# Performance work log

Measured on AMD Instinct MI355X. Metric: run time of the kernel, lower is better.

## Reference

```python
import jax, jax.numpy as jnp
import numpy as np
from jax import lax

B, GRID = 256, 58  # 28*2+2 per scn.InputLayer spatial size


def _conv(x, w):
    # x: [B,C,H,W], w: [O,C,k,k]; scn.Convolution is VALID, stride 1, no bias
    return lax.conv_general_dilated(
        x, w, window_strides=(1, 1), padding='VALID',
        dimension_numbers=('NCHW', 'OIHW', 'NCHW'))


def _maxpool2(x):
    return lax.reduce_window(x, -jnp.inf, lax.max,
                             window_dimensions=(1, 1, 2, 2),
                             window_strides=(1, 1, 2, 2), padding='VALID')


def setup_inputs() -> dict:
    key = jax.random.key(0)
    k0, k1, k2, k3, k4 = jax.random.split(key, 5)
    return {
        'x': jax.random.normal(k0, (B, 1, GRID, GRID), dtype=jnp.float32),
        'w1': jax.random.normal(k1, (64, 1, 5, 5), dtype=jnp.float32) * 0.1,
        'w2': jax.random.normal(k2, (128, 64, 5, 5), dtype=jnp.float32) * 0.025,
        'lw': jax.random.normal(k3, (10, 128), dtype=jnp.float32) * 0.09,
        'lb': jax.random.normal(k4, (10,), dtype=jnp.float32) * 0.01,
    }


def reference(x, w1, w2, lw, lb):
    h = _conv(x, w1)          # [B,64,54,54]
    h = _maxpool2(h)          # [B,64,27,27]
    h = _conv(h, w2)          # [B,128,23,23]
    h = jnp.transpose(h, (0, 2, 3, 1))  # channels-last for linear
    return jnp.einsum('bhwc,oc->bhwo', h, lw) + lb  # [B,23,23,10]
```

## Files before the change

kernel.cpp:

```cpp
#include <hip/hip_runtime.h>


typedef __attribute__((ext_vector_type(8))) short bf16x8;
typedef __attribute__((ext_vector_type(4))) float f32x4;
typedef __attribute__((ext_vector_type(4))) unsigned int u32x4;

#define MFMA16(a, b, c) __builtin_amdgcn_mfma_f32_16x16x32_bf16((a), (b), (c), 0, 0, 0)

static __device__ __forceinline__ unsigned short f2bf(float f) {
    unsigned u = __builtin_bit_cast(unsigned, f);
    u += 0x7FFFu + ((u >> 16) & 1u);
    return (unsigned short)(u >> 16);
}

__global__ __launch_bounds__(256) void prep_w2c(
    const float* __restrict__ w2, unsigned short* __restrict__ w2c)
{
    int t = blockIdx.x * 256 + threadIdx.x;
    if (t >= 25600) return;
    const int lane = t & 63, khalf = (t >> 6) & 1, nt = (t >> 7) & 7, kk = t >> 10;
    const int l16 = lane & 15, kg = lane >> 4;
    const int oc = nt * 16 + l16;
    const int icb = khalf * 32 + kg * 8;
    unsigned pk[4];
#pragma unroll
    for (int h = 0; h < 4; ++h) {
        unsigned short lo = f2bf(w2[oc * 1600 + (icb + 2 * h) * 25 + kk]);
        unsigned short hi = f2bf(w2[oc * 1600 + (icb + 2 * h + 1) * 25 + kk]);
        pk[h] = (unsigned)lo | ((unsigned)hi << 16);
    }
    u32x4 v; v.x = pk[0]; v.y = pk[1]; v.z = pk[2]; v.w = pk[3];
    *(u32x4*)(w2c + (size_t)t * 8) = v;
}

#define XBF_OFF  104976
#define W1T_OFF  111704
#define ECON_STR 272
#define LWT_OFF  147968
#define LDS_TOT  152320

__global__ __launch_bounds__(512, 2) void fused_net(
    const float* __restrict__ x, const float* __restrict__ w1,
    const unsigned short* __restrict__ w2c,
    const float* __restrict__ lw, const float* __restrict__ lb,
    float* __restrict__ out)
{
    extern __shared__ char lds[];
    unsigned short* xbf = (unsigned short*)(lds + XBF_OFF);
    unsigned short* w1t = (unsigned short*)(lds + W1T_OFF);
    const int b = blockIdx.x, tid = threadIdx.x;
    const int lane = tid & 63, w = tid >> 6;
    const int l16 = lane & 15, kg = lane >> 4;
    const int ocg = w & 1, mg = w >> 1;
    const int mstart = (mg == 0) ? 0 : mg * 8 + 1;

    const float4* xg = (const float4*)(x + b * 3364);
    for (int i = tid; i < 841; i += 512) {
        float4 v = xg[i];
        unsigned p0 = (unsigned)f2bf(v.x) | ((unsigned)f2bf(v.y) << 16);
        unsigned p1 = (unsigned)f2bf(v.z) | ((unsigned)f2bf(v.w) << 16);
        *(uint2*)(xbf + i * 4) = make_uint2(p0, p1);
    }
    for (int i = tid; i < 2048; i += 512) {
        int k = i >> 6, oc = i & 63;
        w1t[i] = (k < 25) ? f2bf(w1[oc * 25 + k]) : (unsigned short)0;
    }
    for (int i = tid; i < 2048; i += 512) {
        int o = i >> 7, cc = i & 127;
        float v = (o < 10) ? lw[o * 128 + cc] : 0.f;
        *(unsigned short*)(lds + LWT_OFF + o * 272 + cc * 2) = f2bf(v);
    }
    __syncthreads();

    {
        int koff[8];
        unsigned kmsk[8];
#pragma unroll
        for (int j = 0; j < 8; ++j) {
            int k = kg * 8 + j;
            int kh = k / 5, kw = k - 5 * kh;
            koff[j] = (k < 25) ? (kh * 58 + kw) : 0;
            kmsk[j] = (k < 25) ? 0xFFFFu : 0u;
        }
        bf16x8 bfrag[4];
#pragma unroll
        for (int ot = 0; ot < 4; ++ot)
#pragma unroll
            for (int j = 0; j < 8; ++j)
                bfrag[ot][j] = (short)w1t[(kg * 8 + j) * 64 + ot * 16 + l16];

        const f32x4 zero4 = {0.f, 0.f, 0.f, 0.f};
        for (int t = w; t < 183; t += 8) {
            int p = t * 4 + (l16 >> 2);
            if (p > 728) p = 728;
            const int q = l16 & 3;
            const int ph = p / 27, pw = p - 27 * ph;
            const int base = (2 * ph + (q >> 1)) * 58 + 2 * pw + (q & 1);
            bf16x8 afrag;
#pragma unroll
            for (int j = 0; j < 8; ++j)
                afrag[j] = (short)(xbf[base + koff[j]] & kmsk[j]);
            f32x4 acc1[4];
#pragma unroll
            for (int ot = 0; ot < 4; ++ot)
                acc1[ot] = MFMA16(afrag, bfrag[ot], zero4);
            const int pout = t * 4 + kg;
            if (pout < 729) {
#pragma unroll
                for (int ot = 0; ot < 4; ++ot) {
                    float m = fmaxf(fmaxf(acc1[ot][0], acc1[ot][1]),
                                    fmaxf(acc1[ot][2], acc1[ot][3]));
                    *(unsigned short*)(lds + pout * 144 + (ot * 16 + l16) * 2)
                        = f2bf(m);
                }
            }
        }
    }
    __syncthreads();

    int abase[9];
#pragma unroll
    for (int mt = 0; mt < 9; ++mt) {
        int sp = (mstart + mt) * 16 + l16;
        if (sp > 528) sp = 528;
        int oh = sp / 23, ow = sp - oh * 23;
        abase[mt] = (oh * 27 + ow) * 144 + kg * 16;
    }

    f32x4 acc[9][4];
#pragma unroll
    for (int mt = 0; mt < 9; ++mt)
#pragma unroll
        for (int nt = 0; nt < 4; ++nt)
            acc[mt][nt] = (f32x4){0.f, 0.f, 0.f, 0.f};

    auto loadB = [&](bf16x8* dst, int kkv) {
#pragma unroll
        for (int i = 0; i < 4; ++i) {
#pragma unroll
            for (int hf = 0; hf < 2; ++hf) {
                const int nt = ocg * 4 + i;
                const size_t off =
                    (((size_t)kkv * 8 + nt) * 2 + hf) * 512 + lane * 8;
                dst[i * 2 + hf] = *(const bf16x8*)(w2c + off);
            }
        }
    };
    auto compute = [&](int kkv, const bf16x8* B) {
        const int kh = kkv / 5, kw = kkv - 5 * kh;
        const int pixoffB = (kh * 27 + kw) * 144;
#pragma unroll
        for (int mt = 0; mt < 9; ++mt) {
            const char* ap = lds + abase[mt] + pixoffB;
            bf16x8 a0 = *(const bf16x8*)(ap);
            bf16x8 a1 = *(const bf16x8*)(ap + 64);
#pragma unroll
            for (int i = 0; i < 4; ++i)
                acc[mt][i] = MFMA16(a0, B[i * 2 + 0], acc[mt][i]);
#pragma unroll
            for (int i = 0; i < 4; ++i)
                acc[mt][i] = MFMA16(a1, B[i * 2 + 1], acc[mt][i]);
        }
    };

    bf16x8 bA[8], bB[8];
    loadB(bA, 0);
    for (int kk = 0; kk < 25; kk += 2) {
        if (kk + 1 < 25) loadB(bB, kk + 1);
        compute(kk, bA);
        if (kk + 1 < 25) {
            if (kk + 2 < 25) loadB(bA, kk + 2);
            compute(kk + 1, bB);
        }
    }

    __syncthreads();
    const int oc0 = ocg * 64;
#pragma unroll
    for (int mt = 0; mt < 9; ++mt) {
        const int spb = (mstart + mt) * 16 + kg * 4;
#pragma unroll
        for (int nt = 0; nt < 4; ++nt) {
            const int col = oc0 + nt * 16 + l16;
#pragma unroll
            for (int r = 0; r < 4; ++r) {
                int sp = spb + r;
                if (sp < 529)
                    *(unsigned short*)(lds + sp * ECON_STR + col * 2) =
                        f2bf(acc[mt][nt][r]);
            }
        }
    }
    __syncthreads();

    const float lbv = (l16 < 10) ? lb[l16] : 0.f;
#pragma unroll
    for (int i = 0; i < 5; ++i) {
        const int t = w + 8 * i;
        if (t < 34) {
            f32x4 al = {0.f, 0.f, 0.f, 0.f};
            const char* arow = lds + (t * 16 + l16) * ECON_STR + kg * 16;
            const char* brow = lds + LWT_OFF + l16 * 272 + kg * 16;
#pragma unroll
            for (int ks = 0; ks < 4; ++ks) {
                bf16x8 av = *(const bf16x8*)(arow + ks * 64);
                bf16x8 bv = *(const bf16x8*)(brow + ks * 64);
                al = MFMA16(av, bv, al);
            }
            if (l16 < 10) {
#pragma unroll
                for (int r = 0; r < 4; ++r) {
                    int sp = t * 16 + kg * 4 + r;
                    if (sp < 529)
                        out[((size_t)b * 529 + sp) * 10 + l16] = al[r] + lbv;
                }
            }
        }
    }
}

extern "C" void kernel_launch(void* const* d_in, const int* in_sizes, int n_in,
                              void* d_out, int out_size, void* d_ws, size_t ws_size,
                              hipStream_t stream) {
    const float* x  = (const float*)d_in[0];
    const float* w1 = (const float*)d_in[1];
    const float* w2 = (const float*)d_in[2];
    const float* lw = (const float*)d_in[3];
    const float* lb = (const float*)d_in[4];
    float* out = (float*)d_out;

    unsigned short* w2c = (unsigned short*)d_ws;

    (void)hipFuncSetAttribute((const void*)fused_net,
                              hipFuncAttributeMaxDynamicSharedMemorySize,
                              LDS_TOT);

    prep_w2c<<<100, 256, 0, stream>>>(w2, w2c);
    fused_net<<<256, 512, LDS_TOT, stream>>>(x, w1, w2c, lw, lb, out);
}
```

Baseline: 68.08 us.

## Give each wave all 128 output channels over fewer spatial tiles in conv2

Conv2 work is repartitioned so each wave computes all 8 output-channel tiles for up to 5 spatial M-tiles, instead of 4 channel tiles over 9 M-tiles. Each A fragment read from LDS is reused across 8 MFMAs, and the last tile overlaps (starts at 513) rather than clamping, which removes the padded-row work. The explicit double-buffered B prefetch is dropped: weights are loaded per half-K directly from global/L2, and every wave now reads all of w2c rather than half. This may expose load latency, and the 40 accumulator vectors raise register pressure at 2 blocks per CU.

```diff
diff --git a/kernel.cpp b/kernel.cpp
--- a/kernel.cpp
+++ b/kernel.cpp
@@ -51,8 +51,6 @@
     const int b = blockIdx.x, tid = threadIdx.x;
     const int lane = tid & 63, w = tid >> 6;
     const int l16 = lane & 15, kg = lane >> 4;
-    const int ocg = w & 1, mg = w >> 1;
-    const int mstart = (mg == 0) ? 0 : mg * 8 + 1;
 
     const float4* xg = (const float4*)(x + b * 3364);
     for (int i = tid; i < 841; i += 512) {
@@ -118,76 +116,62 @@
     }
     __syncthreads();
 
-    int abase[9];
-#pragma unroll
-    for (int mt = 0; mt < 9; ++mt) {
-        int sp = (mstart + mt) * 16 + l16;
-        if (sp > 528) sp = 528;
-        int oh = sp / 23, ow = sp - oh * 23;
-        abase[mt] = (oh * 27 + ow) * 144 + kg * 16;
-    }
-
-    f32x4 acc[9][4];
-#pragma unroll
-    for (int mt = 0; mt < 9; ++mt)
-#pragma unroll
-        for (int nt = 0; nt < 4; ++nt)
-            acc[mt][nt] = (f32x4){0.f, 0.f, 0.f, 0.f};
-
-    auto loadB = [&](bf16x8* dst, int kkv) {
-#pragma unroll
-        for (int i = 0; i < 4; ++i) {
-#pragma unroll
-            for (int hf = 0; hf < 2; ++hf) {
-                const int nt = ocg * 4 + i;
-                const size_t off =
-                    (((size_t)kkv * 8 + nt) * 2 + hf) * 512 + lane * 8;
-                dst[i * 2 + hf] = *(const bf16x8*)(w2c + off);
-            }
-        }
-    };
-    auto compute = [&](int kkv, const bf16x8* B) {
-        const int kh = kkv / 5, kw = kkv - 5 * kh;
+    const int mtc = (w < 2) ? 5 : 4;
+    int abase[5];
+#pragma unroll
+    for (int ti = 0; ti < 5; ++ti) {
+        int tile = w + 8 * ti;
+        if (tile > 33) tile = w;
+        const int tstart = (tile == 33) ? 513 : tile * 16;
+        const int sp = tstart + l16;
+        const int oh = sp / 23, ow = sp - oh * 23;
+        abase[ti] = (oh * 27 + ow) * 144 + kg * 16;
+    }
+
+    f32x4 acc[5][8];
+#pragma unroll
+    for (int ti = 0; ti < 5; ++ti)
+#pragma unroll
+        for (int nt = 0; nt < 8; ++nt)
+            acc[ti][nt] = (f32x4){0.f, 0.f, 0.f, 0.f};
+
+    for (int kk = 0; kk < 25; ++kk) {
+        const int kh = kk / 5, kw = kk - 5 * kh;
         const int pixoffB = (kh * 27 + kw) * 144;
-#pragma unroll
-        for (int mt = 0; mt < 9; ++mt) {
-            const char* ap = lds + abase[mt] + pixoffB;
-            bf16x8 a0 = *(const bf16x8*)(ap);
-            bf16x8 a1 = *(const bf16x8*)(ap + 64);
-#pragma unroll
-            for (int i = 0; i < 4; ++i)
-                acc[mt][i] = MFMA16(a0, B[i * 2 + 0], acc[mt][i]);
-#pragma unroll
-            for (int i = 0; i < 4; ++i)
-                acc[mt][i] = MFMA16(a1, B[i * 2 + 1], acc[mt][i]);
-        }
-    };
-
-    bf16x8 bA[8], bB[8];
-    loadB(bA, 0);
-    for (int kk = 0; kk < 25; kk += 2) {
-        if (kk + 1 < 25) loadB(bB, kk + 1);
-        compute(kk, bA);
-        if (kk + 1 < 25) {
-            if (kk + 2 < 25) loadB(bA, kk + 2);
-            compute(kk + 1, bB);
-        }
-    }
-
-    __syncthreads();
-    const int oc0 = ocg * 64;
-#pragma unroll
-    for (int mt = 0; mt < 9; ++mt) {
-        const int spb = (mstart + mt) * 16 + kg * 4;
-#pragma unroll
-        for (int nt = 0; nt < 4; ++nt) {
-            const int col = oc0 + nt * 16 + l16;
-#pragma unroll
-            for (int r = 0; r < 4; ++r) {
-                int sp = spb + r;
-                if (sp < 529)
-                    *(unsigned short*)(lds + sp * ECON_STR + col * 2) =
-                        f2bf(acc[mt][nt][r]);
+        const unsigned short* wp = w2c + (size_t)kk * 8192 + lane * 8;
+#pragma unroll
+        for (int hf = 0; hf < 2; ++hf) {
+            bf16x8 Bf[8];
+#pragma unroll
+            for (int nt = 0; nt < 8; ++nt)
+                Bf[nt] = *(const bf16x8*)(wp + (nt * 2 + hf) * 512);
+#pragma unroll
+            for (int ti = 0; ti < 5; ++ti) {
+                if (ti < mtc) {
+                    bf16x8 a =
+                        *(const bf16x8*)(lds + abase[ti] + pixoffB + hf * 64);
+#pragma unroll
+                    for (int nt = 0; nt < 8; ++nt)
+                        acc[ti][nt] = MFMA16(a, Bf[nt], acc[ti][nt]);
+                }
+            }
+        }
+    }
+
+    __syncthreads();
+#pragma unroll
+    for (int ti = 0; ti < 5; ++ti) {
+        if (ti < mtc) {
+            int tile = w + 8 * ti;
+            if (tile > 33) tile = w;
+            const int rbase = ((tile == 33) ? 513 : tile * 16) + kg * 4;
+#pragma unroll
+            for (int nt = 0; nt < 8; ++nt) {
+                const int col = nt * 16 + l16;
+#pragma unroll
+                for (int r = 0; r < 4; ++r)
+                    *(unsigned short*)(lds + (rbase + r) * ECON_STR + col * 2)
+                        = f2bf(acc[ti][nt][r]);
             }
         }
     }
```

After: 66.04 us. 1.03x faster.
